# Kernel tuning notes

Hardware: AMD Instinct MI355X
Metric: run time of the kernel (lower is better)

## Reference

```python
import jax, jax.numpy as jnp
import numpy as np
from jax import lax

V, E, HD, T = 32000, 256, 256, 4   # vocab, embed dim, lstm hidden (bidir total), tagset (BMES)
H = HD // 2                        # hidden per direction
B, S = 64, 1024


def setup_inputs() -> dict:
    key = jax.random.key(0)
    ks = jax.random.split(key, 16)
    sc = 0.1
    return {
        "sentences": jax.random.randint(ks[0], (B, S), 0, V, dtype=jnp.int32),
        "embed": jax.random.normal(ks[1], (V, E), jnp.float32) * sc,
        "w_ih_f": jax.random.normal(ks[2], (4 * H, E), jnp.float32) * sc,
        "w_hh_f": jax.random.normal(ks[3], (4 * H, H), jnp.float32) * sc,
        "b_ih_f": jax.random.normal(ks[4], (4 * H,), jnp.float32) * sc,
        "b_hh_f": jax.random.normal(ks[5], (4 * H,), jnp.float32) * sc,
        "w_ih_r": jax.random.normal(ks[6], (4 * H, E), jnp.float32) * sc,
        "w_hh_r": jax.random.normal(ks[7], (4 * H, H), jnp.float32) * sc,
        "b_ih_r": jax.random.normal(ks[8], (4 * H,), jnp.float32) * sc,
        "b_hh_r": jax.random.normal(ks[9], (4 * H,), jnp.float32) * sc,
        "w_out": jax.random.normal(ks[10], (T, HD), jnp.float32) * sc,
        "b_out": jax.random.normal(ks[11], (T,), jnp.float32) * sc,
        "start_t": jax.random.normal(ks[12], (T,), jnp.float32) * sc,
        "end_t": jax.random.normal(ks[13], (T,), jnp.float32) * sc,
        "trans": jax.random.normal(ks[14], (T, T), jnp.float32) * sc,
    }


def _lstm_pass(x, w_ih, w_hh, b_ih, b_hh):
    # x: [S, B, E]; PyTorch gate order i, f, g, o; zero initial state.
    bsz = x.shape[1]
    hdim = w_hh.shape[1]
    b = b_ih + b_hh

    def step(carry, xt):
        h, c = carry
        z = xt @ w_ih.T + h @ w_hh.T + b  # [B, 4H]
        i, f, g, o = jnp.split(z, 4, axis=-1)
        c = jax.nn.sigmoid(f) * c + jax.nn.sigmoid(i) * jnp.tanh(g)
        h = jax.nn.sigmoid(o) * jnp.tanh(c)
        return (h, c), h

    init = (jnp.zeros((bsz, hdim), x.dtype), jnp.zeros((bsz, hdim), x.dtype))
    _, hs = lax.scan(step, init, x)
    return hs  # [S, B, H]


def _emissions(sentences, embed, w_ih_f, w_hh_f, b_ih_f, b_hh_f,
               w_ih_r, w_hh_r, b_ih_r, b_hh_r, w_out, b_out):
    x = embed[sentences]                # [B, S, E]
    xs = jnp.transpose(x, (1, 0, 2))    # [S, B, E]
    hf = _lstm_pass(xs, w_ih_f, w_hh_f, b_ih_f, b_hh_f)
    hr = _lstm_pass(xs[::-1], w_ih_r, w_hh_r, b_ih_r, b_hh_r)[::-1]
    h = jnp.concatenate([hf, hr], axis=-1)        # [S, B, 2H]
    return h @ w_out.T + b_out                    # [S, B, T] emissions


def _viterbi_decode(feats, start_t, end_t, trans):
    # feats: [S, B, T] (no mask: all sequences full length, matching crf.decode on dense batch)
    score0 = start_t + feats[0]  # [B, T]

    def fwd_step(score, emit):
        nxt = score[:, :, None] + trans[None, :, :] + emit[:, None, :]  # [B, Tprev, Tcur]
        return jnp.max(nxt, axis=1), jnp.argmax(nxt, axis=1)

    final, bps = lax.scan(fwd_step, score0, feats[1:])  # bps: [S-1, B, T]
    final = final + end_t
    last = jnp.argmax(final, axis=1)  # [B]

    def back_step(tag, bp):
        prev = jnp.take_along_axis(bp, tag[:, None], axis=1)[:, 0]
        return prev, prev

    _, path_head = lax.scan(back_step, last, bps, reverse=True)  # [S-1, B], tags at t=0..S-2
    path = jnp.concatenate([path_head, last[None]], axis=0)      # [S, B]
    return jnp.transpose(path, (1, 0)).astype(jnp.int32)         # [B, S]


def reference(sentences, embed, w_ih_f, w_hh_f, b_ih_f, b_hh_f,
              w_ih_r, w_hh_r, b_ih_r, b_hh_r, w_out, b_out,
              start_t, end_t, trans):
    feats = _emissions(sentences, embed, w_ih_f, w_hh_f, b_ih_f, b_hh_f,
                       w_ih_r, w_hh_r, b_ih_r, b_hh_r, w_out, b_out)
    return _viterbi_decode(feats, start_t, end_t, trans)
```

## Files before the change

kernel.cpp:

```cpp
#include <hip/hip_runtime.h>
#include <cstdint>
#include <cstddef>

#define SLEN 1024
#define BATCH 64
#define EDIM 256
#define HDIM 128
#define GDIM 512
#define NTAG 4
#define VOCAB 32000

typedef float f2 __attribute__((ext_vector_type(2)));
typedef float f4 __attribute__((ext_vector_type(4)));


__device__ __forceinline__ float sigm_f(float x) {
    return 1.0f / (1.0f + __expf(-x));
}
__device__ __forceinline__ float tanh_f(float x) {
    return 1.0f - 2.0f / (1.0f + __expf(2.0f * x));
}

template <int CTRL>
__device__ __forceinline__ float quad_perm(float x) {
    return __int_as_float(
        __builtin_amdgcn_mov_dpp(__float_as_int(x), CTRL, 0xF, 0xF, true));
}
#define QP_XOR1 0xB1
#define QP_XOR2 0x4E
#define QP_MIR8 0x141
#define QP_BC0  0x00
#define QP_BC1  0x55
#define QP_BC2  0xAA
#define QP_BC3  0xFF

__global__ __launch_bounds__(512) void table_k(
    const float* __restrict__ embed,
    const float* __restrict__ w_ih_f, const float* __restrict__ w_ih_r,
    const float* __restrict__ b_ih_f, const float* __restrict__ b_hh_f,
    const float* __restrict__ b_ih_r, const float* __restrict__ b_hh_r,
    float* __restrict__ T)
{
    __shared__ __align__(16) float smem[12288];
    float* As = smem;
    const int t  = threadIdx.x;
    const int tm = t >> 8;
    const int tt = t & 255;
    float* Bs = smem + 4096 + tm * 4096;

    const int mt  = blockIdx.x;
    const int cp  = blockIdx.y;
    const int nt  = cp * 2 + tm;
    const int dir = nt >> 2;
    const float* W  = dir ? w_ih_r : w_ih_f;
    const float* bi = dir ? b_ih_r : b_ih_f;
    const float* bh = dir ? b_hh_r : b_hh_f;
    const int ncol = (nt & 3) * 128;
    const int r0   = mt * 128;

    const int sra = t & 127;
    const int qa  = t >> 7;
    const float* arow = embed + (size_t)(r0 + sra) * EDIM + qa * 8;

    const int srb = tt & 127;
    const int hb  = tt >> 7;
    const float* brow = W + (size_t)(ncol + srb) * EDIM + hb * 16;

    const int tx = tt & 15, ty = tt >> 4;

    f2 acc[8][4];
    #pragma unroll
    for (int i = 0; i < 8; ++i)
        #pragma unroll
        for (int jj = 0; jj < 4; ++jj) acc[i][jj] = (f2)(0.0f);

    for (int kt = 0; kt < 8; ++kt) {
        const int k0 = kt * 32;
        __syncthreads();
        {
            float4 v0 = *(const float4*)(arow + k0);
            float4 v1 = *(const float4*)(arow + k0 + 4);
            const int kk = qa * 8;
            As[(kk + 0) * 128 + sra] = v0.x;
            As[(kk + 1) * 128 + sra] = v0.y;
            As[(kk + 2) * 128 + sra] = v0.z;
            As[(kk + 3) * 128 + sra] = v0.w;
            As[(kk + 4) * 128 + sra] = v1.x;
            As[(kk + 5) * 128 + sra] = v1.y;
            As[(kk + 6) * 128 + sra] = v1.z;
            As[(kk + 7) * 128 + sra] = v1.w;
        }
        #pragma unroll
        for (int i = 0; i < 4; ++i) {
            float4 v = *(const float4*)(brow + k0 + i * 4);
            const int kk = hb * 16 + i * 4;
            Bs[(kk + 0) * 128 + srb] = v.x;
            Bs[(kk + 1) * 128 + srb] = v.y;
            Bs[(kk + 2) * 128 + srb] = v.z;
            Bs[(kk + 3) * 128 + srb] = v.w;
        }
        __syncthreads();

        #pragma unroll 8
        for (int k = 0; k < 32; ++k) {
            const f4 a0  = *(const f4*)&As[k * 128 + ty * 4];
            const f4 a1  = *(const f4*)&As[k * 128 + 64 + ty * 4];
            const f4 bq0 = *(const f4*)&Bs[k * 128 + tx * 4];
            const f4 bq1 = *(const f4*)&Bs[k * 128 + 64 + tx * 4];
            float av[8] = {a0.x, a0.y, a0.z, a0.w, a1.x, a1.y, a1.z, a1.w};
            f2 bv[4];
            bv[0] = __builtin_shufflevector(bq0, bq0, 0, 1);
            bv[1] = __builtin_shufflevector(bq0, bq0, 2, 3);
            bv[2] = __builtin_shufflevector(bq1, bq1, 0, 1);
            bv[3] = __builtin_shufflevector(bq1, bq1, 2, 3);
            #pragma unroll
            for (int i = 0; i < 8; ++i) {
                f2 as; as.x = av[i]; as.y = av[i];
                #pragma unroll
                for (int jj = 0; jj < 4; ++jj)
                    acc[i][jj] += as * bv[jj];
            }
        }
    }

    float bias0[4], bias1[4];
    #pragma unroll
    for (int j = 0; j < 4; ++j) {
        bias0[j] = bi[ncol + tx * 4 + j] + bh[ncol + tx * 4 + j];
        bias1[j] = bi[ncol + 64 + tx * 4 + j] + bh[ncol + 64 + tx * 4 + j];
    }

    #pragma unroll
    for (int i = 0; i < 8; ++i) {
        const int row = r0 + ((i < 4) ? (ty * 4 + i) : (64 + ty * 4 + i - 4));
        float* zp = T + (size_t)row * 1024 + dir * 512 + ncol;
        float4 o0, o1;
        o0.x = acc[i][0].x + bias0[0]; o0.y = acc[i][0].y + bias0[1];
        o0.z = acc[i][1].x + bias0[2]; o0.w = acc[i][1].y + bias0[3];
        o1.x = acc[i][2].x + bias1[0]; o1.y = acc[i][2].y + bias1[1];
        o1.z = acc[i][3].x + bias1[2]; o1.w = acc[i][3].y + bias1[3];
        *(float4*)(zp + tx * 4)      = o0;
        *(float4*)(zp + 64 + tx * 4) = o1;
    }
}

__global__ __launch_bounds__(512) __attribute__((amdgpu_waves_per_eu(2, 2)))
void lstm_k(
    const float* __restrict__ T, const int* __restrict__ sent,
    const float* __restrict__ w_hh_f, const float* __restrict__ w_hh_r,
    float* __restrict__ H)
{
    __shared__ __align__(16) float sh_h[320];
    __shared__ int sh_tok[SLEN];

    const int bid = blockIdx.x;
    const int b   = bid & 63;
    const int dir = bid >> 6;
    const int q   = threadIdx.x;
    const int p   = q & 7;
    const int Q   = q >> 3;
    const int gt  = p & 3;
    const int hi  = p >> 2;
    const int u   = Q + hi * 64;

    const float* Whh = dir ? w_hh_r : w_hh_f;

    f2 w2[8][8];
    #pragma unroll
    for (int pr = 0; pr < 8; ++pr) {
        const int uu = (pr & 4) ? (Q + 64) : Q;
        const int gg = pr & 3;
        const f2* src =
            (const f2*)(Whh + ((size_t)(gg * 128 + uu) * 128 + p * 16));
        #pragma unroll
        for (int i = 0; i < 8; ++i) w2[pr][i] = src[i];
    }
    #pragma unroll
    for (int pr = 0; pr < 8; ++pr)
        #pragma unroll
        for (int i = 0; i < 8; ++i)
            asm volatile("" : "+v"(w2[pr][i]));

    sh_tok[q]       = sent[b * SLEN + q];
    sh_tok[512 + q] = sent[b * SLEN + 512 + q];
    if (q < 128) sh_h[(q >> 5) * 36 + (q & 31)] = 0.0f;
    float c = 0.0f;
    __syncthreads();

    const int zcol = dir * 512 + gt * 128 + u;
    const ptrdiff_t hstride = dir ? -16384 : 16384;
    float* hg = H + ((size_t)(dir ? (SLEN - 1) : 0) * 64 + b) * 256
              + dir * 128 + u;

    const bool k4 = (p & 4) != 0;
    const bool k2 = (p & 2) != 0;
    const bool k1 = (p & 1) != 0;
    const float gsc  = (gt == 2) ? 2.0f : 1.0f;
    const float gofs = (gt == 2) ? -1.0f : 0.0f;
    const int shr = (p >> 1) * 36 + (p & 1) * 16;
    const int shw = (u >> 5) * 36 + (u & 31);

    float zcur[4], znxt[4];
    #pragma unroll
    for (int dt = 0; dt < 4; ++dt) {
        const int s = dir ? (SLEN - 1 - dt) : dt;
        zcur[dt] = T[((size_t)sh_tok[s] << 10) + zcol];
    }

    for (int t0 = 0; t0 < SLEN; t0 += 4) {
        const bool more = (t0 + 4 < SLEN);
        if (more) {
            #pragma unroll
            for (int dt = 0; dt < 4; ++dt) {
                const int tn = t0 + 4 + dt;
                const int s = dir ? (SLEN - 1 - tn) : tn;
                znxt[dt] = T[((size_t)sh_tok[s] << 10) + zcol];
            }
        }

        #pragma unroll
        for (int dt = 0; dt < 4; ++dt) {
            const f4* hp = (const f4*)(sh_h + (dt & 1) * 160 + shr);
            f2 hv[8];
            #pragma unroll
            for (int i = 0; i < 4; ++i) {
                f4 v = hp[i];
                hv[2 * i]     = __builtin_shufflevector(v, v, 0, 1);
                hv[2 * i + 1] = __builtin_shufflevector(v, v, 2, 3);
            }
            float s[8];
            #pragma unroll
            for (int pr = 0; pr < 8; ++pr) {
                f2 a = (f2)(0.0f);
                #pragma unroll
                for (int i = 0; i < 8; ++i) a += w2[pr][i] * hv[i];
                s[pr] = a.x + a.y;
            }
            float K1[4];
            #pragma unroll
            for (int j = 0; j < 4; ++j) {
                float keep = k4 ? s[j + 4] : s[j];
                float send = k4 ? s[j] : s[j + 4];
                K1[j] = keep + quad_perm<QP_MIR8>(send);
            }
            float K2[2];
            #pragma unroll
            for (int j = 0; j < 2; ++j) {
                float keep = k2 ? K1[j + 2] : K1[j];
                float send = k2 ? K1[j] : K1[j + 2];
                K2[j] = keep + quad_perm<QP_XOR2>(send);
            }
            float keep3 = k1 ? K2[1] : K2[0];
            float send3 = k1 ? K2[0] : K2[1];
            float zv = keep3 + quad_perm<QP_XOR1>(send3) + zcur[dt];

            float sgv = sigm_f(zv * gsc);
            float act = fmaf(sgv, gsc, gofs);

            float a_i = quad_perm<QP_BC0>(act);
            float a_f = quad_perm<QP_BC1>(act);
            float a_g = quad_perm<QP_BC2>(act);
            float a_o = quad_perm<QP_BC3>(act);
            c = a_f * c + a_i * a_g;
            float h = a_o * tanh_f(c);

            if (gt == 0) {
                sh_h[((dt + 1) & 1) * 160 + shw] = h;
                *hg = h;
            }
            hg += hstride;
            __syncthreads();
        }

        if (more) {
            #pragma unroll
            for (int dt = 0; dt < 4; ++dt) zcur[dt] = znxt[dt];
        }
    }
}

__device__ __forceinline__ void gemm_body(
    float* smem, int mt, int cp,
    const int* __restrict__ sent, const float* __restrict__ embed,
    const float* __restrict__ w_ih_f, const float* __restrict__ w_ih_r,
    const float* __restrict__ b_ih_f, const float* __restrict__ b_hh_f,
    const float* __restrict__ b_ih_r, const float* __restrict__ b_hh_r,
    float* __restrict__ Z, int base_f, int base_r)
{
    float* As = smem;
    const int t  = threadIdx.x;
    const int tm = t >> 8;
    const int tt = t & 255;
    float* Bs = smem + 4096 + tm * 4096;

    const int nt  = cp * 2 + tm;
    const int dir = nt >> 2;
    const float* W  = dir ? w_ih_r : w_ih_f;
    const float* bi = dir ? b_ih_r : b_ih_f;
    const float* bh = dir ? b_hh_r : b_hh_f;
    const int ncol = (nt & 3) * 128;
    const int r0   = mt * 128;

    const int sra = t & 127;
    const int qa  = t >> 7;
    const int r_loc = r0 + sra;
    const int s_loc = r_loc >> 6;
    const int b_    = r_loc & 63;
    const int s_glob = (dir ? base_r : base_f) + s_loc;
    const int tok = sent[b_ * SLEN + s_glob];
    const float* arow = embed + (size_t)tok * EDIM + qa * 8;

    const int srb = tt & 127;
    const int hb  = tt >> 7;
    const float* brow = W + (size_t)(ncol + srb) * EDIM + hb * 16;

    const int tx = tt & 15, ty = tt >> 4;

    f2 acc[8][4];
    #pragma unroll
    for (int i = 0; i < 8; ++i)
        #pragma unroll
        for (int jj = 0; jj < 4; ++jj) acc[i][jj] = (f2)(0.0f);

    for (int kt = 0; kt < 8; ++kt) {
        const int k0 = kt * 32;
        __syncthreads();
        {
            float4 v0 = *(const float4*)(arow + k0);
            float4 v1 = *(const float4*)(arow + k0 + 4);
            const int kk = qa * 8;
            As[(kk + 0) * 128 + sra] = v0.x;
            As[(kk + 1) * 128 + sra] = v0.y;
            As[(kk + 2) * 128 + sra] = v0.z;
            As[(kk + 3) * 128 + sra] = v0.w;
            As[(kk + 4) * 128 + sra] = v1.x;
            As[(kk + 5) * 128 + sra] = v1.y;
            As[(kk + 6) * 128 + sra] = v1.z;
            As[(kk + 7) * 128 + sra] = v1.w;
        }
        #pragma unroll
        for (int i = 0; i < 4; ++i) {
            float4 v = *(const float4*)(brow + k0 + i * 4);
            const int kk = hb * 16 + i * 4;
            Bs[(kk + 0) * 128 + srb] = v.x;
            Bs[(kk + 1) * 128 + srb] = v.y;
            Bs[(kk + 2) * 128 + srb] = v.z;
            Bs[(kk + 3) * 128 + srb] = v.w;
        }
        __syncthreads();

        #pragma unroll 8
        for (int k = 0; k < 32; ++k) {
            const f4 a0  = *(const f4*)&As[k * 128 + ty * 4];
            const f4 a1  = *(const f4*)&As[k * 128 + 64 + ty * 4];
            const f4 bq0 = *(const f4*)&Bs[k * 128 + tx * 4];
            const f4 bq1 = *(const f4*)&Bs[k * 128 + 64 + tx * 4];
            float av[8] = {a0.x, a0.y, a0.z, a0.w, a1.x, a1.y, a1.z, a1.w};
            f2 bv[4];
            bv[0] = __builtin_shufflevector(bq0, bq0, 0, 1);
            bv[1] = __builtin_shufflevector(bq0, bq0, 2, 3);
            bv[2] = __builtin_shufflevector(bq1, bq1, 0, 1);
            bv[3] = __builtin_shufflevector(bq1, bq1, 2, 3);
            #pragma unroll
            for (int i = 0; i < 8; ++i) {
                f2 as; as.x = av[i]; as.y = av[i];
                #pragma unroll
                for (int jj = 0; jj < 4; ++jj)
                    acc[i][jj] += as * bv[jj];
            }
        }
    }

    float bias0[4], bias1[4];
    #pragma unroll
    for (int j = 0; j < 4; ++j) {
        bias0[j] = bi[ncol + tx * 4 + j] + bh[ncol + tx * 4 + j];
        bias1[j] = bi[ncol + 64 + tx * 4 + j] + bh[ncol + 64 + tx * 4 + j];
    }

    #pragma unroll
    for (int i = 0; i < 8; ++i) {
        const int row = r0 + ((i < 4) ? (ty * 4 + i) : (64 + ty * 4 + i - 4));
        float* zp = Z + (size_t)row * 1024 + dir * 512 + ncol;
        float4 o0, o1;
        o0.x = acc[i][0].x + bias0[0]; o0.y = acc[i][0].y + bias0[1];
        o0.z = acc[i][1].x + bias0[2]; o0.w = acc[i][1].y + bias0[3];
        o1.x = acc[i][2].x + bias1[0]; o1.y = acc[i][2].y + bias1[1];
        o1.z = acc[i][3].x + bias1[2]; o1.w = acc[i][3].y + bias1[3];
        *(float4*)(zp + tx * 4)      = o0;
        *(float4*)(zp + 64 + tx * 4) = o1;
    }
}

__device__ __forceinline__ void lstm_body(
    float* smem,
    const float* __restrict__ Z, const float* __restrict__ w_hh_f,
    const float* __restrict__ w_hh_r, float* __restrict__ H,
    float* __restrict__ ST, int base_f, int base_r, int L, int first)
{
    float* sh_h = smem;

    const int bid = blockIdx.x;
    const int b   = bid & 63;
    const int dir = bid >> 6;
    const int q   = threadIdx.x;
    const int p   = q & 7;
    const int Q   = q >> 3;
    const int gt  = p & 3;
    const int hi  = p >> 2;
    const int u   = Q + hi * 64;

    const float* Whh = dir ? w_hh_r : w_hh_f;

    f2 w2[8][8];
    #pragma unroll
    for (int pr = 0; pr < 8; ++pr) {
        const int uu = (pr & 4) ? (Q + 64) : Q;
        const int gg = pr & 3;
        const f2* src =
            (const f2*)(Whh + ((size_t)(gg * 128 + uu) * 128 + p * 16));
        #pragma unroll
        for (int i = 0; i < 8; ++i) w2[pr][i] = src[i];
    }

    float* stp = ST + (size_t)(dir * 64 + b) * 256;
    if (q < 128)
        sh_h[(q >> 5) * 36 + (q & 31)] = first ? 0.0f : stp[q];
    float c = first ? 0.0f : stp[128 + u];

    const ptrdiff_t zstride = dir ? -65536 : 65536;
    const float* zp0 = Z + (size_t)b * 1024 + dir * 512
                     + (dir ? (size_t)(L - 1) * 65536 : 0) + gt * 128 + u;
    const ptrdiff_t hstride = dir ? -16384 : 16384;
    float* hg = H + ((size_t)(dir ? (base_r + L - 1) : base_f) * 64 + b) * 256
              + dir * 128 + u;

    const bool k4 = (p & 4) != 0;
    const bool k2 = (p & 2) != 0;
    const bool k1 = (p & 1) != 0;
    const float gsc  = (gt == 2) ? 2.0f : 1.0f;
    const float gofs = (gt == 2) ? -1.0f : 0.0f;
    const int shr = (p >> 1) * 36 + (p & 1) * 16;
    const int shw = (u >> 5) * 36 + (u & 31);

    float zcur[4], znxt[4];
    {
        const float* zp = zp0;
        #pragma unroll
        for (int dt = 0; dt < 4; ++dt) { zcur[dt] = *zp; zp += zstride; }
    }
    __syncthreads();

    float hlast = 0.0f;

    for (int t0 = 0; t0 < L; t0 += 4) {
        const bool more = (t0 + 4 < L);
        if (more) {
            const float* zp = zp0 + (ptrdiff_t)(t0 + 4) * zstride;
            #pragma unroll
            for (int dt = 0; dt < 4; ++dt) { znxt[dt] = *zp; zp += zstride; }
        }

        #pragma unroll
        for (int dt = 0; dt < 4; ++dt) {
            const f4* hp = (const f4*)(sh_h + (dt & 1) * 160 + shr);
            f2 hv[8];
            #pragma unroll
            for (int i = 0; i < 4; ++i) {
                f4 v = hp[i];
                hv[2 * i]     = __builtin_shufflevector(v, v, 0, 1);
                hv[2 * i + 1] = __builtin_shufflevector(v, v, 2, 3);
            }
            float s[8];
            #pragma unroll
            for (int pr = 0; pr < 8; ++pr) {
                f2 a = (f2)(0.0f);
                #pragma unroll
                for (int i = 0; i < 8; ++i) a += w2[pr][i] * hv[i];
                s[pr] = a.x + a.y;
            }
            float K1[4];
            #pragma unroll
            for (int j = 0; j < 4; ++j) {
                float keep = k4 ? s[j + 4] : s[j];
                float send = k4 ? s[j] : s[j + 4];
                K1[j] = keep + quad_perm<QP_MIR8>(send);
            }
            float K2[2];
            #pragma unroll
            for (int j = 0; j < 2; ++j) {
                float keep = k2 ? K1[j + 2] : K1[j];
                float send = k2 ? K1[j] : K1[j + 2];
                K2[j] = keep + quad_perm<QP_XOR2>(send);
            }
            float keep3 = k1 ? K2[1] : K2[0];
            float send3 = k1 ? K2[0] : K2[1];
            float zv = keep3 + quad_perm<QP_XOR1>(send3) + zcur[dt];

            float sgv = sigm_f(zv * gsc);
            float act = fmaf(sgv, gsc, gofs);

            float a_i = quad_perm<QP_BC0>(act);
            float a_f = quad_perm<QP_BC1>(act);
            float a_g = quad_perm<QP_BC2>(act);
            float a_o = quad_perm<QP_BC3>(act);
            c = a_f * c + a_i * a_g;
            float h = a_o * tanh_f(c);
            hlast = h;

            if (gt == 0) {
                sh_h[((dt + 1) & 1) * 160 + shw] = h;
                *hg = h;
            }
            hg += hstride;
            __syncthreads();
        }

        if (more) {
            #pragma unroll
            for (int dt = 0; dt < 4; ++dt) zcur[dt] = znxt[dt];
        }
    }

    if (gt == 0) {
        stp[u] = hlast;
        stp[128 + u] = c;
    }
}

__global__ __launch_bounds__(512) void fused_lstm_gemm(
    const int* __restrict__ sent, const float* __restrict__ embed,
    const float* __restrict__ w_ih_f, const float* __restrict__ w_ih_r,
    const float* __restrict__ b_ih_f, const float* __restrict__ b_hh_f,
    const float* __restrict__ b_ih_r, const float* __restrict__ b_hh_r,
    float* __restrict__ Zw, int gbase_f, int gbase_r, int mtiles,
    const float* __restrict__ Zr, const float* __restrict__ w_hh_f,
    const float* __restrict__ w_hh_r, float* __restrict__ H,
    float* __restrict__ ST, int lbase_f, int lbase_r, int L, int first)
{
    __shared__ __align__(16) float smem[12288];

    if (blockIdx.x < 128) {
        lstm_body(smem, Zr, w_hh_f, w_hh_r, H, ST, lbase_f, lbase_r, L, first);
    } else {
        const int g  = blockIdx.x - 128;
        const int mt = g % mtiles;
        const int cp = g / mtiles;
        gemm_body(smem, mt, cp, sent, embed, w_ih_f, w_ih_r,
                  b_ih_f, b_hh_f, b_ih_r, b_hh_r, Zw, gbase_f, gbase_r);
    }
}

__global__ __launch_bounds__(512) void gemm_zin(
    const int* __restrict__ sent, const float* __restrict__ embed,
    const float* __restrict__ w_ih_f, const float* __restrict__ w_ih_r,
    const float* __restrict__ b_ih_f, const float* __restrict__ b_hh_f,
    const float* __restrict__ b_ih_r, const float* __restrict__ b_hh_r,
    float* __restrict__ Z, int base_f, int base_r)
{
    __shared__ __align__(16) float smem[12288];
    gemm_body(smem, blockIdx.x, blockIdx.y, sent, embed, w_ih_f, w_ih_r,
              b_ih_f, b_hh_f, b_ih_r, b_hh_r, Z, base_f, base_r);
}

__global__ __launch_bounds__(256) void emissions_k(
    const float* __restrict__ H, const float* __restrict__ w_out,
    const float* __restrict__ b_out, float* __restrict__ F)
{
    const int gid = blockIdx.x * 256 + threadIdx.x;
    const int r   = gid >> 2;
    const int tg  = gid & 3;
    const float4* h4 = (const float4*)(H + (size_t)r * 256);
    const float4* w4 = (const float4*)(w_out + (size_t)tg * 256);
    float a0 = 0.f, a1 = 0.f, a2 = 0.f, a3 = 0.f;
    #pragma unroll 8
    for (int k = 0; k < 64; ++k) {
        float4 h = h4[k], w = w4[k];
        a0 = fmaf(h.x, w.x, a0); a1 = fmaf(h.y, w.y, a1);
        a2 = fmaf(h.z, w.z, a2); a3 = fmaf(h.w, w.w, a3);
    }
    F[gid] = ((a0 + a1) + (a2 + a3)) + b_out[tg];
}

__device__ __forceinline__ unsigned compose_map(unsigned a, unsigned b) {
    unsigned r = 0;
    #pragma unroll
    for (int jj = 0; jj < 4; ++jj) {
        unsigned bj = (b >> (jj * 8)) & 3u;
        unsigned aj = (a >> (bj * 8)) & 3u;
        r |= aj << (jj * 8);
    }
    return r;
}

__global__ __launch_bounds__(64) void viterbi_k(
    const float* __restrict__ F, const float* __restrict__ start_t,
    const float* __restrict__ end_t, const float* __restrict__ trans,
    int* __restrict__ out)
{
    const int b    = blockIdx.x;
    const int lane = threadIdx.x;
    __shared__ __align__(16) float sfeat[SLEN][NTAG];
    __shared__ unsigned sbp[SLEN];

    #pragma unroll
    for (int i = 0; i < 16; ++i) {
        int s = i * 64 + lane;
        ((float4*)sfeat)[s] = *(const float4*)(F + ((size_t)s * BATCH + b) * NTAG);
    }
    __syncthreads();

    const int cur = lane & 3;
    float tr0 = trans[0 * 4 + cur], tr1 = trans[1 * 4 + cur];
    float tr2 = trans[2 * 4 + cur], tr3 = trans[3 * 4 + cur];
    float sc = start_t[cur] + sfeat[0][cur];

    for (int s = 1; s < SLEN; ++s) {
        float ft = sfeat[s][cur];
        float s0 = __shfl(sc, 0), s1 = __shfl(sc, 1);
        float s2 = __shfl(sc, 2), s3 = __shfl(sc, 3);
        float c0 = s0 + tr0, c1 = s1 + tr1, c2 = s2 + tr2, c3 = s3 + tr3;
        float best = c0; int arg = 0;
        if (c1 > best) { best = c1; arg = 1; }
        if (c2 > best) { best = c2; arg = 2; }
        if (c3 > best) { best = c3; arg = 3; }
        sc = best + ft;
        unsigned bp = (unsigned)arg;
        unsigned b0 = __shfl(bp, 0), b1 = __shfl(bp, 1);
        unsigned b2 = __shfl(bp, 2), b3 = __shfl(bp, 3);
        if (lane == 0) sbp[s] = b0 | (b1 << 8) | (b2 << 16) | (b3 << 24);
    }
    sc += end_t[cur];
    float f0 = __shfl(sc, 0), f1 = __shfl(sc, 1);
    float f2v = __shfl(sc, 2), f3 = __shfl(sc, 3);
    int last = 0; float bb = f0;
    if (f1 > bb)  { bb = f1;  last = 1; }
    if (f2v > bb) { bb = f2v; last = 2; }
    if (f3 > bb)  { bb = f3;  last = 3; }
    __syncthreads();

    unsigned m[16];
    #pragma unroll
    for (int k = 0; k < 16; ++k) {
        int s = lane * 16 + k;
        m[k] = (s >= 1) ? sbp[s] : 0x03020100u;
    }
    unsigned G = m[15];
    #pragma unroll
    for (int k = 14; k >= 0; --k) G = compose_map(m[k], G);
    unsigned R = G;
    #pragma unroll
    for (int d = 1; d < 64; d <<= 1) {
        unsigned oo = __shfl_down(R, d);
        if (lane + d < 64) R = compose_map(R, oo);
    }
    unsigned P = __shfl_down(R, 1);
    if (lane == 63) P = 0x03020100u;

    int tcur = (int)((P >> (last * 8)) & 3u);
    int* ob = out + b * SLEN + lane * 16;
    ob[15] = tcur;
    #pragma unroll
    for (int k = 15; k >= 1; --k) {
        tcur = (int)((m[k] >> (tcur * 8)) & 3u);
        ob[k - 1] = tcur;
    }
}

extern "C" void kernel_launch(void* const* d_in, const int* in_sizes, int n_in,
                              void* d_out, int out_size, void* d_ws, size_t ws_size,
                              hipStream_t stream)
{
    const int*   sent    = (const int*)d_in[0];
    const float* embed   = (const float*)d_in[1];
    const float* w_ih_f  = (const float*)d_in[2];
    const float* w_hh_f  = (const float*)d_in[3];
    const float* b_ih_f  = (const float*)d_in[4];
    const float* b_hh_f  = (const float*)d_in[5];
    const float* w_ih_r  = (const float*)d_in[6];
    const float* w_hh_r  = (const float*)d_in[7];
    const float* b_ih_r  = (const float*)d_in[8];
    const float* b_hh_r  = (const float*)d_in[9];
    const float* w_out   = (const float*)d_in[10];
    const float* b_out   = (const float*)d_in[11];
    const float* start_t = (const float*)d_in[12];
    const float* end_t   = (const float*)d_in[13];
    const float* trans   = (const float*)d_in[14];
    int* out = (int*)d_out;

    const size_t H_FLOATS  = (size_t)SLEN * BATCH * 256;
    const size_t F_FLOATS  = (size_t)SLEN * BATCH * NTAG;
    const size_t T_FLOATS  = (size_t)VOCAB * 1024;
    const size_t ST_FLOATS = (size_t)2 * BATCH * 256;

    const size_t table_need = (T_FLOATS + H_FLOATS + F_FLOATS) * sizeof(float);

    if (ws_size >= table_need) {
        float* T = (float*)d_ws;
        float* H = T + T_FLOATS;
        float* F = H + H_FLOATS;

        table_k<<<dim3(250, 4), 512, 0, stream>>>(
            embed, w_ih_f, w_ih_r, b_ih_f, b_hh_f, b_ih_r, b_hh_r, T);
        lstm_k<<<128, 512, 0, stream>>>(T, sent, w_hh_f, w_hh_r, H);
        emissions_k<<<1024, 256, 0, stream>>>(H, w_out, b_out, F);
        viterbi_k<<<64, 64, 0, stream>>>(F, start_t, end_t, trans, out);
        return;
    }

    const size_t FIXED = H_FLOATS + F_FLOATS + ST_FLOATS;
    int L = 0;
    for (int cand = 256; cand >= 32; cand >>= 1) {
        size_t need = ((size_t)2 * cand * BATCH * 1024 + FIXED) * sizeof(float);
        if (need <= ws_size) { L = cand; break; }
    }

    if (L > 0) {
        const int nch = SLEN / L;
        const int mtiles = (L * BATCH) / 128;
        float* Z0 = (float*)d_ws;
        float* Z1 = Z0 + (size_t)L * BATCH * 1024;
        float* H  = Z1 + (size_t)L * BATCH * 1024;
        float* F  = H + H_FLOATS;
        float* ST = F + F_FLOATS;
        float* Zb[2] = {Z0, Z1};

        gemm_zin<<<dim3(mtiles, 4), 512, 0, stream>>>(
            sent, embed, w_ih_f, w_ih_r, b_ih_f, b_hh_f, b_ih_r, b_hh_r,
            Zb[0], 0, SLEN - L);

        for (int c = 0; c < nch; ++c) {
            const int lbase_f = c * L;
            const int lbase_r = SLEN - (c + 1) * L;
            const int hasg = (c + 1 < nch);
            const int gbase_f = (c + 1) * L;
            const int gbase_r = SLEN - (c + 2) * L;
            const int grid = hasg ? (128 + mtiles * 4) : 128;
            fused_lstm_gemm<<<grid, 512, 0, stream>>>(
                sent, embed, w_ih_f, w_ih_r, b_ih_f, b_hh_f, b_ih_r, b_hh_r,
                Zb[(c + 1) & 1], hasg ? gbase_f : 0, hasg ? gbase_r : 0, mtiles,
                Zb[c & 1], w_hh_f, w_hh_r, H, ST, lbase_f, lbase_r, L,
                c == 0 ? 1 : 0);
        }

        emissions_k<<<1024, 256, 0, stream>>>(H, w_out, b_out, F);
        viterbi_k<<<64, 64, 0, stream>>>(F, start_t, end_t, trans, out);
    } else {
        int Ls = SLEN;
        while (Ls > 32) {
            size_t need = ((size_t)Ls * BATCH * 1024 + FIXED) * sizeof(float);
            if (need <= ws_size) break;
            Ls >>= 1;
        }
        const int nch = SLEN / Ls;
        const int mtiles = (Ls * BATCH) / 128;
        float* Z  = (float*)d_ws;
        float* H  = Z + (size_t)Ls * BATCH * 1024;
        float* F  = H + H_FLOATS;
        float* ST = F + F_FLOATS;

        for (int c = 0; c < nch; ++c) {
            const int base_f = c * Ls;
            const int base_r = SLEN - (c + 1) * Ls;
            gemm_zin<<<dim3(mtiles, 4), 512, 0, stream>>>(
                sent, embed, w_ih_f, w_ih_r, b_ih_f, b_hh_f, b_ih_r, b_hh_r,
                Z, base_f, base_r);
            fused_lstm_gemm<<<128, 512, 0, stream>>>(
                sent, embed, w_ih_f, w_ih_r, b_ih_f, b_hh_f, b_ih_r, b_hh_r,
                Z, 0, 0, mtiles,
                Z, w_hh_f, w_hh_r, H, ST, base_f, base_r, Ls, c == 0 ? 1 : 0);
        }
        emissions_k<<<1024, 256, 0, stream>>>(H, w_out, b_out, F);
        viterbi_k<<<64, 64, 0, stream>>>(F, start_t, end_t, trans, out);
    }
}
```

Measured before the change: 1.122 ms.

## Restructure vocab-gate table GEMM to per-wave column strips with scalar weight loads

Replaces the 128x128 shared-memory register-tiled GEMM that builds the vocab-by-gate input projection table with a simpler scheme. Each block stages a 64-row embedding tile in LDS and each wave computes 16 output columns per lane-row, reading weights straight from global memory as wave-uniform loads. The grid grows to 500x8 blocks. This cuts LDS traffic and register pressure and may raise occupancy, but each embedding element is reused across far fewer columns, so arithmetic intensity drops and more global and cache traffic is needed for weights.

```diff
diff --git a/kernel.cpp b/kernel.cpp
--- a/kernel.cpp
+++ b/kernel.cpp
@@ -41,106 +41,64 @@
     const float* __restrict__ b_ih_r, const float* __restrict__ b_hh_r,
     float* __restrict__ T)
 {
-    __shared__ __align__(16) float smem[12288];
-    float* As = smem;
-    const int t  = threadIdx.x;
-    const int tm = t >> 8;
-    const int tt = t & 255;
-    float* Bs = smem + 4096 + tm * 4096;
-
-    const int mt  = blockIdx.x;
-    const int cp  = blockIdx.y;
-    const int nt  = cp * 2 + tm;
-    const int dir = nt >> 2;
-    const float* W  = dir ? w_ih_r : w_ih_f;
+    __shared__ __align__(16) float As[64 * 20];
+
+    const int t    = threadIdx.x;
+    const int lane = t & 63;
+    const int w    = __builtin_amdgcn_readfirstlane(t >> 6);
+    const int rowbase = blockIdx.x * 64;
+    const int row  = rowbase + lane;
+    const int gcol = blockIdx.y * 128 + w * 16;
+    const int dir  = gcol >> 9;
+    const int c0   = gcol & 511;
+
+    const float* Wd = dir ? w_ih_r : w_ih_f;
     const float* bi = dir ? b_ih_r : b_ih_f;
     const float* bh = dir ? b_hh_r : b_hh_f;
-    const int ncol = (nt & 3) * 128;
-    const int r0   = mt * 128;
-
-    const int sra = t & 127;
-    const int qa  = t >> 7;
-    const float* arow = embed + (size_t)(r0 + sra) * EDIM + qa * 8;
-
-    const int srb = tt & 127;
-    const int hb  = tt >> 7;
-    const float* brow = W + (size_t)(ncol + srb) * EDIM + hb * 16;
-
-    const int tx = tt & 15, ty = tt >> 4;
-
-    f2 acc[8][4];
-    #pragma unroll
-    for (int i = 0; i < 8; ++i)
-        #pragma unroll
-        for (int jj = 0; jj < 4; ++jj) acc[i][jj] = (f2)(0.0f);
-
-    for (int kt = 0; kt < 8; ++kt) {
-        const int k0 = kt * 32;
+
+    float acc[16];
+    #pragma unroll
+    for (int c = 0; c < 16; ++c) acc[c] = 0.0f;
+
+    for (int kt = 0; kt < 16; ++kt) {
+        const int k0 = kt * 16;
         __syncthreads();
-        {
-            float4 v0 = *(const float4*)(arow + k0);
-            float4 v1 = *(const float4*)(arow + k0 + 4);
-            const int kk = qa * 8;
-            As[(kk + 0) * 128 + sra] = v0.x;
-            As[(kk + 1) * 128 + sra] = v0.y;
-            As[(kk + 2) * 128 + sra] = v0.z;
-            As[(kk + 3) * 128 + sra] = v0.w;
-            As[(kk + 4) * 128 + sra] = v1.x;
-            As[(kk + 5) * 128 + sra] = v1.y;
-            As[(kk + 6) * 128 + sra] = v1.z;
-            As[(kk + 7) * 128 + sra] = v1.w;
-        }
-        #pragma unroll
-        for (int i = 0; i < 4; ++i) {
-            float4 v = *(const float4*)(brow + k0 + i * 4);
-            const int kk = hb * 16 + i * 4;
-            Bs[(kk + 0) * 128 + srb] = v.x;
-            Bs[(kk + 1) * 128 + srb] = v.y;
-            Bs[(kk + 2) * 128 + srb] = v.z;
-            Bs[(kk + 3) * 128 + srb] = v.w;
+        if (t < 256) {
+            const int r = t >> 2, e = t & 3;
+            const float4 v = *(const float4*)(
+                embed + (size_t)(rowbase + r) * EDIM + k0 + e * 4);
+            *(float4*)(As + r * 20 + e * 4) = v;
         }
         __syncthreads();
 
-        #pragma unroll 8
-        for (int k = 0; k < 32; ++k) {
-            const f4 a0  = *(const f4*)&As[k * 128 + ty * 4];
-            const f4 a1  = *(const f4*)&As[k * 128 + 64 + ty * 4];
-            const f4 bq0 = *(const f4*)&Bs[k * 128 + tx * 4];
-            const f4 bq1 = *(const f4*)&Bs[k * 128 + 64 + tx * 4];
-            float av[8] = {a0.x, a0.y, a0.z, a0.w, a1.x, a1.y, a1.z, a1.w};
-            f2 bv[4];
-            bv[0] = __builtin_shufflevector(bq0, bq0, 0, 1);
-            bv[1] = __builtin_shufflevector(bq0, bq0, 2, 3);
-            bv[2] = __builtin_shufflevector(bq1, bq1, 0, 1);
-            bv[3] = __builtin_shufflevector(bq1, bq1, 2, 3);
-            #pragma unroll
-            for (int i = 0; i < 8; ++i) {
-                f2 as; as.x = av[i]; as.y = av[i];
-                #pragma unroll
-                for (int jj = 0; jj < 4; ++jj)
-                    acc[i][jj] += as * bv[jj];
-            }
-        }
-    }
-
-    float bias0[4], bias1[4];
+        const f4 a0 = *(const f4*)(As + lane * 20);
+        const f4 a1 = *(const f4*)(As + lane * 20 + 4);
+        const f4 a2 = *(const f4*)(As + lane * 20 + 8);
+        const f4 a3 = *(const f4*)(As + lane * 20 + 12);
+        const float ar[16] = {a0.x, a0.y, a0.z, a0.w,
+                              a1.x, a1.y, a1.z, a1.w,
+                              a2.x, a2.y, a2.z, a2.w,
+                              a3.x, a3.y, a3.z, a3.w};
+
+        #pragma unroll
+        for (int c = 0; c < 16; ++c) {
+            const float* wr = Wd + (size_t)(c0 + c) * EDIM + k0;
+            #pragma unroll
+            for (int k = 0; k < 16; ++k)
+                acc[c] = fmaf(wr[k], ar[k], acc[c]);
+        }
+    }
+
+    #pragma unroll
+    for (int c = 0; c < 16; ++c) acc[c] += bi[c0 + c] + bh[c0 + c];
+
+    float* tp = T + (size_t)row * 1024 + gcol;
     #pragma unroll
     for (int j = 0; j < 4; ++j) {
-        bias0[j] = bi[ncol + tx * 4 + j] + bh[ncol + tx * 4 + j];
-        bias1[j] = bi[ncol + 64 + tx * 4 + j] + bh[ncol + 64 + tx * 4 + j];
-    }
-
-    #pragma unroll
-    for (int i = 0; i < 8; ++i) {
-        const int row = r0 + ((i < 4) ? (ty * 4 + i) : (64 + ty * 4 + i - 4));
-        float* zp = T + (size_t)row * 1024 + dir * 512 + ncol;
-        float4 o0, o1;
-        o0.x = acc[i][0].x + bias0[0]; o0.y = acc[i][0].y + bias0[1];
-        o0.z = acc[i][1].x + bias0[2]; o0.w = acc[i][1].y + bias0[3];
-        o1.x = acc[i][2].x + bias1[0]; o1.y = acc[i][2].y + bias1[1];
-        o1.z = acc[i][3].x + bias1[2]; o1.w = acc[i][3].y + bias1[3];
-        *(float4*)(zp + tx * 4)      = o0;
-        *(float4*)(zp + 64 + tx * 4) = o1;
+        f4 o;
+        o.x = acc[j * 4 + 0]; o.y = acc[j * 4 + 1];
+        o.z = acc[j * 4 + 2]; o.w = acc[j * 4 + 3];
+        *(f4*)(tp + j * 4) = o;
     }
 }
 
@@ -700,7 +658,7 @@
         float* H = T + T_FLOATS;
         float* F = H + H_FLOATS;
 
-        table_k<<<dim3(250, 4), 512, 0, stream>>>(
+        table_k<<<dim3(500, 8), 512, 0, stream>>>(
             embed, w_ih_f, w_ih_r, b_ih_f, b_hh_f, b_ih_r, b_hh_r, T);
         lstm_k<<<128, 512, 0, stream>>>(T, sent, w_hh_f, w_hh_r, H);
         emissions_k<<<1024, 256, 0, stream>>>(H, w_out, b_out, F);
```

New measurement: 1.264 ms. 1.13x slower.
